# Performance work log

Measured on AMD Instinct MI355X. Metric: run time of the kernel, lower is better.

## Reference

```python
import jax, jax.numpy as jnp
import numpy as np

B, N, OUT = 128, 4096, 64
PHI = (64, 128, 256)
RHO = (256, 128)
FMIN = jnp.finfo(jnp.float32).min


def _linear_params(key, fan_in, fan_out):
    # torch nn.Linear default init: U(-1/sqrt(fan_in), 1/sqrt(fan_in))
    kw, kb = jax.random.split(key)
    bound = 1.0 / np.sqrt(fan_in)
    w = jax.random.uniform(kw, (fan_in, fan_out), jnp.float32, -bound, bound)
    b = jax.random.uniform(kb, (fan_out,), jnp.float32, -bound, bound)
    return w, b


def setup_inputs() -> dict:
    key = jax.random.key(0)
    ks = jax.random.split(key, 8)
    points = jax.random.normal(ks[0], (B, N, 2), jnp.float32)
    lengths = jax.random.randint(ks[1], (B,), 1, N + 1, jnp.int32)
    w1, b1 = _linear_params(ks[2], 2, PHI[0])
    w2, b2 = _linear_params(ks[3], PHI[0], PHI[1])
    w3, b3 = _linear_params(ks[4], PHI[1], PHI[2])
    r1w, r1b = _linear_params(ks[5], PHI[2], RHO[0])
    r2w, r2b = _linear_params(ks[6], RHO[0], RHO[1])
    r3w, r3b = _linear_params(ks[7], RHO[1], OUT)
    return {"points": points, "lengths": lengths,
            "w1": w1, "b1": b1, "w2": w2, "b2": b2, "w3": w3, "b3": b3,
            "r1w": r1w, "r1b": r1b, "r2w": r2w, "r2b": r2b, "r3w": r3w, "r3b": r3b}


def reference(points, lengths, w1, b1, w2, b2, w3, b3, r1w, r1b, r2w, r2b, r3w, r3b):
    # mask[b, n] = n < lengths[b]   (pad_sequence equivalent)
    mask = jnp.arange(N)[None, :] < lengths[:, None]            # [B, N]
    # phi MLP: per-point 2 -> 64 -> 128 -> 256 with ReLU
    h = jax.nn.relu(jnp.einsum('bnd,df->bnf', points, w1) + b1)
    h = jax.nn.relu(jnp.einsum('bnd,df->bnf', h, w2) + b2)
    h = jax.nn.relu(jnp.einsum('bnd,df->bnf', h, w3) + b3)       # [B, N, 256]
    # masked max-pool over points (padding -> dtype min, matching masked_fill)
    h = jnp.where(mask[:, :, None], h, FMIN)
    agg = jnp.max(h, axis=1)                                     # [B, 256]
    # rho MLP: 256 -> 256 -> 128 -> OUT (ReLU on hidden layers only)
    z = jax.nn.relu(agg @ r1w + r1b)
    z = jax.nn.relu(z @ r2w + r2b)
    return z @ r3w + r3b                                         # [B, OUT]
```

## Files before the change

### kernel.cpp

```cpp
#include <hip/hip_runtime.h>
#include <hip/hip_fp16.h>

#define BB   128
#define NN   4096
#define OUTD 64
#define P1   64
#define P2   128
#define P3   256
#define R1   256
#define R2   128
#define CHUNK 64

typedef _Float16 half8 __attribute__((ext_vector_type(8)));
typedef _Float16 half4 __attribute__((ext_vector_type(4)));
typedef float    f32x4 __attribute__((ext_vector_type(4)));

#define AGG_OFF 0
#define W2F_OFF (BB * P3 * 4)
#define W3F_OFF (W2F_OFF + P2 * P1 * 2)

__global__ void prep_kernel(const float* __restrict__ w2, const float* __restrict__ w3,
                            unsigned char* ws) {
  int idx = blockIdx.x * 256 + threadIdx.x;
  if (idx < BB * P3) ((unsigned*)(ws + AGG_OFF))[idx] = 0u;
  _Float16* W2F = (_Float16*)(ws + W2F_OFF);
  _Float16* W3F = (_Float16*)(ws + W3F_OFF);
  if (idx < P1 * P2) {
    int f = idx >> 9, rem = idx & 511, l = rem >> 3, j = rem & 7;
    int mt = f >> 1, ks = f & 1;
    int ch = mt * 16 + (l & 15), k = ks * 32 + (l >> 4) * 8 + j;
    W2F[idx] = (_Float16)w2[k * P2 + ch];
  }
  int i2 = idx - P1 * P2;
  if (i2 >= 0 && i2 < P2 * P3) {
    int f = i2 >> 9, rem = i2 & 511, l = rem >> 3, j = rem & 7;
    int mt = f >> 2, ks = f & 3;
    int ch = mt * 16 + (l & 15), k = ks * 32 + (l >> 4) * 8 + j;
    W3F[i2] = (_Float16)w3[k * P3 + ch];
  }
}

__launch_bounds__(256, 3)
__global__ void phi_kernel(const float* __restrict__ pts, const int* __restrict__ lengths,
                           const float* __restrict__ w1, const float* __restrict__ b1,
                           const float* __restrict__ b2, const float* __restrict__ b3,
                           unsigned char* ws) {
  __shared__ __align__(16) _Float16 sH1[8][CHUNK][8];
  __shared__ __align__(16) _Float16 sH2[16][CHUNK][8];

  int b  = blockIdx.y;
  int c0 = blockIdx.x * CHUNK;
  int len = lengths[b];
  if (c0 >= len) return;
  int v = min(CHUNK, len - c0);

  int t = threadIdx.x;
  int w = t >> 6, l = t & 63;
  int ml = l & 15, q = l >> 4;

  const half8* W2F = (const half8*)(ws + W2F_OFF);
  const half8* W3F = (const half8*)(ws + W3F_OFF);

  half8 a2[2][2];
#pragma unroll
  for (int mt2 = 0; mt2 < 2; ++mt2)
#pragma unroll
    for (int ks = 0; ks < 2; ++ks)
      a2[mt2][ks] = W2F[((w * 2 + mt2) * 2 + ks) * 64 + l];
  half8 a3c[4];
#pragma unroll
  for (int ks = 0; ks < 4; ++ks)
    a3c[ks] = W3F[((w * 4 + 0) * 4 + ks) * 64 + l];

  {
    const float2* Pp = (const float2*)pts + (size_t)b * NN + c0;
    float2 xy = Pp[l];
    half8 h8[2];
#pragma unroll
    for (int j = 0; j < 16; ++j) {
      int jj = w * 16 + j;
      float h = fmaf(xy.y, w1[P1 + jj], fmaf(xy.x, w1[jj], b1[jj]));
      h8[j >> 3][j & 7] = (_Float16)fmaxf(h, 0.f);
    }
    *(half8*)&sH1[w * 2][l][0]     = h8[0];
    *(half8*)&sH1[w * 2 + 1][l][0] = h8[1];
  }
  __syncthreads();

  {
    f32x4 acc2[2][4] = {};
#pragma unroll
    for (int ks = 0; ks < 2; ++ks) {
      half8 bf[4];
#pragma unroll
      for (int nt = 0; nt < 4; ++nt)
        bf[nt] = *(const half8*)&sH1[ks * 4 + q][nt * 16 + ml][0];
#pragma unroll
      for (int mt2 = 0; mt2 < 2; ++mt2)
#pragma unroll
        for (int nt = 0; nt < 4; ++nt)
          acc2[mt2][nt] = __builtin_amdgcn_mfma_f32_16x16x32_f16(
              a2[mt2][ks], bf[nt], acc2[mt2][nt], 0, 0, 0);
    }
#pragma unroll
    for (int mt2 = 0; mt2 < 2; ++mt2) {
      float4 b2v = *(const float4*)&b2[(w * 2 + mt2) * 16 + q * 4];
#pragma unroll
      for (int nt = 0; nt < 4; ++nt) {
        half4 hp;
        hp[0] = (_Float16)fmaxf(acc2[mt2][nt][0] + b2v.x, 0.f);
        hp[1] = (_Float16)fmaxf(acc2[mt2][nt][1] + b2v.y, 0.f);
        hp[2] = (_Float16)fmaxf(acc2[mt2][nt][2] + b2v.z, 0.f);
        hp[3] = (_Float16)fmaxf(acc2[mt2][nt][3] + b2v.w, 0.f);
        *(half4*)&sH2[(w * 2 + mt2) * 2 + (q >> 1)][nt * 16 + ml][(q & 1) * 4] = hp;
      }
    }
  }
  __syncthreads();

  unsigned* aggU = (unsigned*)(ws + AGG_OFF) + b * P3;
  half8 bf3[4][4];
#pragma unroll
  for (int ks = 0; ks < 4; ++ks)
#pragma unroll
    for (int nt = 0; nt < 4; ++nt)
      bf3[ks][nt] = *(const half8*)&sH2[ks * 4 + q][nt * 16 + ml][0];

  for (int s = 0; s < 4; ++s) {
    float4 b3v = *(const float4*)&b3[(w * 4 + s) * 16 + q * 4];
    f32x4 acc3[4] = {};
#pragma unroll
    for (int ks = 0; ks < 4; ++ks)
#pragma unroll
      for (int nt = 0; nt < 4; ++nt)
        acc3[nt] = __builtin_amdgcn_mfma_f32_16x16x32_f16(
            a3c[ks], bf3[ks][nt], acc3[nt], 0, 0, 0);
    if (s < 3) {
#pragma unroll
      for (int ks = 0; ks < 4; ++ks)
        a3c[ks] = W3F[((w * 4 + s + 1) * 4 + ks) * 64 + l];
    }
    float rm[4] = {0.f, 0.f, 0.f, 0.f};
    float bb[4] = {b3v.x, b3v.y, b3v.z, b3v.w};
#pragma unroll
    for (int nt = 0; nt < 4; ++nt) {
      bool ok = (nt * 16 + ml) < v;
#pragma unroll
      for (int r = 0; r < 4; ++r) {
        float val = fmaxf(acc3[nt][r] + bb[r], 0.f);
        if (ok) rm[r] = fmaxf(rm[r], val);
      }
    }
#pragma unroll
    for (int r = 0; r < 4; ++r) {
      float m = rm[r];
      m = fmaxf(m, __shfl_xor(m, 1));
      m = fmaxf(m, __shfl_xor(m, 2));
      m = fmaxf(m, __shfl_xor(m, 4));
      m = fmaxf(m, __shfl_xor(m, 8));
      if (ml == 0)
        atomicMax(&aggU[(w * 4 + s) * 16 + q * 4 + r], __float_as_uint(m));
    }
  }
}

__global__ void rho_kernel(const unsigned char* __restrict__ ws,
                           const float* __restrict__ r1w, const float* __restrict__ r1b,
                           const float* __restrict__ r2w, const float* __restrict__ r2b,
                           const float* __restrict__ r3w, const float* __restrict__ r3b,
                           float* __restrict__ out) {
  __shared__ float sa[R1], sz1[R1], sz2[R2];
  int b = blockIdx.x, t = threadIdx.x;
  const float* agg = (const float*)(ws + AGG_OFF) + b * P3;
  sa[t] = agg[t];
  __syncthreads();
  {
    float p0 = 0.f, p1 = 0.f, p2 = 0.f, p3 = 0.f;
#pragma unroll 8
    for (int k = 0; k < 64; ++k) {
      p0 = fmaf(sa[k],       r1w[k * R1 + t],         p0);
      p1 = fmaf(sa[k + 64],  r1w[(k + 64) * R1 + t],  p1);
      p2 = fmaf(sa[k + 128], r1w[(k + 128) * R1 + t], p2);
      p3 = fmaf(sa[k + 192], r1w[(k + 192) * R1 + t], p3);
    }
    sz1[t] = fmaxf(r1b[t] + ((p0 + p1) + (p2 + p3)), 0.f);
  }
  __syncthreads();
  if (t < R2) {
    float p0 = 0.f, p1 = 0.f, p2 = 0.f, p3 = 0.f;
#pragma unroll 8
    for (int k = 0; k < 64; ++k) {
      p0 = fmaf(sz1[k],       r2w[k * R2 + t],         p0);
      p1 = fmaf(sz1[k + 64],  r2w[(k + 64) * R2 + t],  p1);
      p2 = fmaf(sz1[k + 128], r2w[(k + 128) * R2 + t], p2);
      p3 = fmaf(sz1[k + 192], r2w[(k + 192) * R2 + t], p3);
    }
    sz2[t] = fmaxf(r2b[t] + ((p0 + p1) + (p2 + p3)), 0.f);
  }
  __syncthreads();
  if (t < OUTD) {
    float p0 = 0.f, p1 = 0.f;
#pragma unroll 8
    for (int k = 0; k < 64; ++k) {
      p0 = fmaf(sz2[k],      r3w[k * OUTD + t],        p0);
      p1 = fmaf(sz2[k + 64], r3w[(k + 64) * OUTD + t], p1);
    }
    out[b * OUTD + t] = r3b[t] + p0 + p1;
  }
}

extern "C" void kernel_launch(void* const* d_in, const int* in_sizes, int n_in,
                              void* d_out, int out_size, void* d_ws, size_t ws_size,
                              hipStream_t stream) {
  const float* pts     = (const float*)d_in[0];
  const int*   lengths = (const int*)d_in[1];
  const float* w1  = (const float*)d_in[2];
  const float* b1  = (const float*)d_in[3];
  const float* w2  = (const float*)d_in[4];
  const float* b2  = (const float*)d_in[5];
  const float* w3  = (const float*)d_in[6];
  const float* b3  = (const float*)d_in[7];
  const float* r1w = (const float*)d_in[8];
  const float* r1b = (const float*)d_in[9];
  const float* r2w = (const float*)d_in[10];
  const float* r2b = (const float*)d_in[11];
  const float* r3w = (const float*)d_in[12];
  const float* r3b = (const float*)d_in[13];
  unsigned char* ws = (unsigned char*)d_ws;

  prep_kernel<<<160, 256, 0, stream>>>(w2, w3, ws);
  phi_kernel<<<dim3(NN / CHUNK, BB), 256, 0, stream>>>(pts, lengths, w1, b1, b2, b3, ws);
  rho_kernel<<<BB, 256, 0, stream>>>(ws, r1w, r1b, r2w, r2b, r3w, r3b, (float*)d_out);
}
```

Measured before the change: 142.3 us.

## Process four point chunks per block with software-pipelined layer-1 and W3 prefetch

Each phi block now loops over up to four 64-point chunks instead of one. This amortizes the W2 fragment loads, launch overhead and block setup across more work. Inside the loop, the next chunk's points are loaded and its layer-1 activations computed while the current chunk's layer-3 MFMAs run, and W3 fragments are double-buffered into a second register set. The trade-off is four times fewer blocks (lower parallelism and load balance across ragged lengths), more register pressure from a3n, and an extra barrier per chunk.

```diff
diff --git a/kernel.cpp b/kernel.cpp
--- a/kernel.cpp
+++ b/kernel.cpp
@@ -10,6 +10,7 @@
 #define R1   256
 #define R2   128
 #define CHUNK 64
+#define NCH  4
 
 typedef _Float16 half8 __attribute__((ext_vector_type(8)));
 typedef _Float16 half4 __attribute__((ext_vector_type(4)));
@@ -48,11 +49,12 @@
   __shared__ __align__(16) _Float16 sH1[8][CHUNK][8];
   __shared__ __align__(16) _Float16 sH2[16][CHUNK][8];
 
-  int b  = blockIdx.y;
-  int c0 = blockIdx.x * CHUNK;
-  int len = lengths[b];
-  if (c0 >= len) return;
-  int v = min(CHUNK, len - c0);
+  int b    = blockIdx.y;
+  int base = blockIdx.x * (CHUNK * NCH);
+  int len  = lengths[b];
+  if (base >= len) return;
+  int rem  = len - base;
+  int nch  = min(NCH, (rem + CHUNK - 1) >> 6);
 
   int t = threadIdx.x;
   int w = t >> 6, l = t & 63;
@@ -60,6 +62,7 @@
 
   const half8* W2F = (const half8*)(ws + W2F_OFF);
   const half8* W3F = (const half8*)(ws + W3F_OFF);
+  const float2* Pp = (const float2*)pts + (size_t)b * NN + base;
 
   half8 a2[2][2];
 #pragma unroll
@@ -67,14 +70,15 @@
 #pragma unroll
     for (int ks = 0; ks < 2; ++ks)
       a2[mt2][ks] = W2F[((w * 2 + mt2) * 2 + ks) * 64 + l];
-  half8 a3c[4];
+  half8 a3c[4], a3n[4];
 #pragma unroll
   for (int ks = 0; ks < 4; ++ks)
     a3c[ks] = W3F[((w * 4 + 0) * 4 + ks) * 64 + l];
 
+  float2 xy = Pp[l];
+  unsigned* aggU = (unsigned*)(ws + AGG_OFF) + b * P3;
+
   {
-    const float2* Pp = (const float2*)pts + (size_t)b * NN + c0;
-    float2 xy = Pp[l];
     half8 h8[2];
 #pragma unroll
     for (int j = 0; j < 16; ++j) {
@@ -87,80 +91,104 @@
   }
   __syncthreads();
 
-  {
-    f32x4 acc2[2][4] = {};
-#pragma unroll
-    for (int ks = 0; ks < 2; ++ks) {
-      half8 bf[4];
+  for (int c = 0; c < nch; ++c) {
+    bool more = (c + 1 < nch);
+    if (more) xy = Pp[(c + 1) * CHUNK + l];
+
+    {
+      f32x4 acc2[2][4] = {};
+#pragma unroll
+      for (int ks = 0; ks < 2; ++ks) {
+        half8 bf[4];
+#pragma unroll
+        for (int nt = 0; nt < 4; ++nt)
+          bf[nt] = *(const half8*)&sH1[ks * 4 + q][nt * 16 + ml][0];
+#pragma unroll
+        for (int mt2 = 0; mt2 < 2; ++mt2)
+#pragma unroll
+          for (int nt = 0; nt < 4; ++nt)
+            acc2[mt2][nt] = __builtin_amdgcn_mfma_f32_16x16x32_f16(
+                a2[mt2][ks], bf[nt], acc2[mt2][nt], 0, 0, 0);
+      }
+#pragma unroll
+      for (int mt2 = 0; mt2 < 2; ++mt2) {
+        float4 b2v = *(const float4*)&b2[(w * 2 + mt2) * 16 + q * 4];
+#pragma unroll
+        for (int nt = 0; nt < 4; ++nt) {
+          half4 hp;
+          hp[0] = (_Float16)fmaxf(acc2[mt2][nt][0] + b2v.x, 0.f);
+          hp[1] = (_Float16)fmaxf(acc2[mt2][nt][1] + b2v.y, 0.f);
+          hp[2] = (_Float16)fmaxf(acc2[mt2][nt][2] + b2v.z, 0.f);
+          hp[3] = (_Float16)fmaxf(acc2[mt2][nt][3] + b2v.w, 0.f);
+          *(half4*)&sH2[(w * 2 + mt2) * 2 + (q >> 1)][nt * 16 + ml][(q & 1) * 4] = hp;
+        }
+      }
+    }
+    __syncthreads();
+
+    half8 bf3[4][4];
+#pragma unroll
+    for (int ks = 0; ks < 4; ++ks)
 #pragma unroll
       for (int nt = 0; nt < 4; ++nt)
-        bf[nt] = *(const half8*)&sH1[ks * 4 + q][nt * 16 + ml][0];
-#pragma unroll
-      for (int mt2 = 0; mt2 < 2; ++mt2)
+        bf3[ks][nt] = *(const half8*)&sH2[ks * 4 + q][nt * 16 + ml][0];
+
+    if (more) {
+      half8 h8[2];
+#pragma unroll
+      for (int j = 0; j < 16; ++j) {
+        int jj = w * 16 + j;
+        float h = fmaf(xy.y, w1[P1 + jj], fmaf(xy.x, w1[jj], b1[jj]));
+        h8[j >> 3][j & 7] = (_Float16)fmaxf(h, 0.f);
+      }
+      *(half8*)&sH1[w * 2][l][0]     = h8[0];
+      *(half8*)&sH1[w * 2 + 1][l][0] = h8[1];
+    }
+
+    int v = min(CHUNK, len - base - c * CHUNK);
+#pragma unroll
+    for (int s = 0; s < 4; ++s) {
+      bool pf = (s < 3) || more;
+      if (pf) {
+#pragma unroll
+        for (int ks = 0; ks < 4; ++ks)
+          a3n[ks] = W3F[((w * 4 + ((s + 1) & 3)) * 4 + ks) * 64 + l];
+      }
+      float4 b3v = *(const float4*)&b3[(w * 4 + s) * 16 + q * 4];
+      f32x4 acc3[4] = {};
+#pragma unroll
+      for (int ks = 0; ks < 4; ++ks)
 #pragma unroll
         for (int nt = 0; nt < 4; ++nt)
-          acc2[mt2][nt] = __builtin_amdgcn_mfma_f32_16x16x32_f16(
-              a2[mt2][ks], bf[nt], acc2[mt2][nt], 0, 0, 0);
-    }
-#pragma unroll
-    for (int mt2 = 0; mt2 < 2; ++mt2) {
-      float4 b2v = *(const float4*)&b2[(w * 2 + mt2) * 16 + q * 4];
+          acc3[nt] = __builtin_amdgcn_mfma_f32_16x16x32_f16(
+              a3c[ks], bf3[ks][nt], acc3[nt], 0, 0, 0);
+      float rm[4] = {0.f, 0.f, 0.f, 0.f};
+      float bb[4] = {b3v.x, b3v.y, b3v.z, b3v.w};
 #pragma unroll
       for (int nt = 0; nt < 4; ++nt) {
-        half4 hp;
-        hp[0] = (_Float16)fmaxf(acc2[mt2][nt][0] + b2v.x, 0.f);
-        hp[1] = (_Float16)fmaxf(acc2[mt2][nt][1] + b2v.y, 0.f);
-        hp[2] = (_Float16)fmaxf(acc2[mt2][nt][2] + b2v.z, 0.f);
-        hp[3] = (_Float16)fmaxf(acc2[mt2][nt][3] + b2v.w, 0.f);
-        *(half4*)&sH2[(w * 2 + mt2) * 2 + (q >> 1)][nt * 16 + ml][(q & 1) * 4] = hp;
-      }
-    }
-  }
-  __syncthreads();
-
-  unsigned* aggU = (unsigned*)(ws + AGG_OFF) + b * P3;
-  half8 bf3[4][4];
-#pragma unroll
-  for (int ks = 0; ks < 4; ++ks)
-#pragma unroll
-    for (int nt = 0; nt < 4; ++nt)
-      bf3[ks][nt] = *(const half8*)&sH2[ks * 4 + q][nt * 16 + ml][0];
-
-  for (int s = 0; s < 4; ++s) {
-    float4 b3v = *(const float4*)&b3[(w * 4 + s) * 16 + q * 4];
-    f32x4 acc3[4] = {};
-#pragma unroll
-    for (int ks = 0; ks < 4; ++ks)
-#pragma unroll
-      for (int nt = 0; nt < 4; ++nt)
-        acc3[nt] = __builtin_amdgcn_mfma_f32_16x16x32_f16(
-            a3c[ks], bf3[ks][nt], acc3[nt], 0, 0, 0);
-    if (s < 3) {
-#pragma unroll
-      for (int ks = 0; ks < 4; ++ks)
-        a3c[ks] = W3F[((w * 4 + s + 1) * 4 + ks) * 64 + l];
-    }
-    float rm[4] = {0.f, 0.f, 0.f, 0.f};
-    float bb[4] = {b3v.x, b3v.y, b3v.z, b3v.w};
-#pragma unroll
-    for (int nt = 0; nt < 4; ++nt) {
-      bool ok = (nt * 16 + ml) < v;
+        bool ok = (nt * 16 + ml) < v;
+#pragma unroll
+        for (int r = 0; r < 4; ++r) {
+          float val = fmaxf(acc3[nt][r] + bb[r], 0.f);
+          if (ok) rm[r] = fmaxf(rm[r], val);
+        }
+      }
 #pragma unroll
       for (int r = 0; r < 4; ++r) {
-        float val = fmaxf(acc3[nt][r] + bb[r], 0.f);
-        if (ok) rm[r] = fmaxf(rm[r], val);
-      }
-    }
-#pragma unroll
-    for (int r = 0; r < 4; ++r) {
-      float m = rm[r];
-      m = fmaxf(m, __shfl_xor(m, 1));
-      m = fmaxf(m, __shfl_xor(m, 2));
-      m = fmaxf(m, __shfl_xor(m, 4));
-      m = fmaxf(m, __shfl_xor(m, 8));
-      if (ml == 0)
-        atomicMax(&aggU[(w * 4 + s) * 16 + q * 4 + r], __float_as_uint(m));
-    }
+        float m = rm[r];
+        m = fmaxf(m, __shfl_xor(m, 1));
+        m = fmaxf(m, __shfl_xor(m, 2));
+        m = fmaxf(m, __shfl_xor(m, 4));
+        m = fmaxf(m, __shfl_xor(m, 8));
+        if (ml == 0)
+          atomicMax(&aggU[(w * 4 + s) * 16 + q * 4 + r], __float_as_uint(m));
+      }
+      if (pf) {
+#pragma unroll
+        for (int ks = 0; ks < 4; ++ks) a3c[ks] = a3n[ks];
+      }
+    }
+    __syncthreads();
   }
 }
 
@@ -229,6 +257,6 @@
   unsigned char* ws = (unsigned char*)d_ws;
 
   prep_kernel<<<160, 256, 0, stream>>>(w2, w3, ws);
-  phi_kernel<<<dim3(NN / CHUNK, BB), 256, 0, stream>>>(pts, lengths, w1, b1, b2, b3, ws);
+  phi_kernel<<<dim3(NN / (CHUNK * NCH), BB), 256, 0, stream>>>(pts, lengths, w1, b1, b2, b3, ws);
   rho_kernel<<<BB, 256, 0, stream>>>(ws, r1w, r1b, r2w, r2b, r3w, r3b, (float*)d_out);
 }
```

Result: slower. 265.4 us (+86.5%).

## Make phi kernel persistent per batch with strided chunks and register max accumulation

Applied to the files above, without the earlier changes.

Replaces the one-block-per-chunk grid with a fixed grid of six blocks per batch row. Each block loops over chunks with stride six, keeps the running max in registers across chunks, and issues atomicMax once at the end. It also prefetches the next chunk's points and drops the ReLU on the last layer, since the running max starts at zero. This is meant to cut atomics, block launch overhead and repeated weight loads. In exchange there is more register pressure, and load balance across blocks now depends on the sequence lengths.

```diff
diff --git a/kernel.cpp b/kernel.cpp
--- a/kernel.cpp
+++ b/kernel.cpp
@@ -10,6 +10,9 @@
 #define R1   256
 #define R2   128
 #define CHUNK 64
+#define NCHK (NN / CHUNK)
+#define GPB  6
+#define PGRID (BB * GPB)
 
 typedef _Float16 half8 __attribute__((ext_vector_type(8)));
 typedef _Float16 half4 __attribute__((ext_vector_type(4)));
@@ -48,11 +51,10 @@
   __shared__ __align__(16) _Float16 sH1[8][CHUNK][8];
   __shared__ __align__(16) _Float16 sH2[16][CHUNK][8];
 
-  int b  = blockIdx.y;
-  int c0 = blockIdx.x * CHUNK;
+  int bid = blockIdx.x;
+  int b = bid & (BB - 1), g = bid >> 7;
   int len = lengths[b];
-  if (c0 >= len) return;
-  int v = min(CHUNK, len - c0);
+  if (g * CHUNK >= len) return;
 
   int t = threadIdx.x;
   int w = t >> 6, l = t & 63;
@@ -60,6 +62,8 @@
 
   const half8* W2F = (const half8*)(ws + W2F_OFF);
   const half8* W3F = (const half8*)(ws + W3F_OFF);
+  const float2* Pp = (const float2*)pts + (size_t)b * NN;
+  unsigned* aggU = (unsigned*)(ws + AGG_OFF) + b * P3;
 
   half8 a2[2][2];
 #pragma unroll
@@ -72,88 +76,96 @@
   for (int ks = 0; ks < 4; ++ks)
     a3c[ks] = W3F[((w * 4 + 0) * 4 + ks) * 64 + l];
 
-  {
-    const float2* Pp = (const float2*)pts + (size_t)b * NN + c0;
-    float2 xy = Pp[l];
-    half8 h8[2];
-#pragma unroll
-    for (int j = 0; j < 16; ++j) {
-      int jj = w * 16 + j;
-      float h = fmaf(xy.y, w1[P1 + jj], fmaf(xy.x, w1[jj], b1[jj]));
-      h8[j >> 3][j & 7] = (_Float16)fmaxf(h, 0.f);
-    }
-    *(half8*)&sH1[w * 2][l][0]     = h8[0];
-    *(half8*)&sH1[w * 2 + 1][l][0] = h8[1];
-  }
-  __syncthreads();
-
-  {
-    f32x4 acc2[2][4] = {};
-#pragma unroll
-    for (int ks = 0; ks < 2; ++ks) {
-      half8 bf[4];
+  float2 xy = Pp[g * CHUNK + l];
+
+  float rm[4][4] = {};
+
+  for (int c = g; c * CHUNK < len; c += GPB) {
+    int v = min(CHUNK, len - c * CHUNK);
+
+    {
+      half8 h8[2];
+#pragma unroll
+      for (int j = 0; j < 16; ++j) {
+        int jj = w * 16 + j;
+        float h = fmaf(xy.y, w1[P1 + jj], fmaf(xy.x, w1[jj], b1[jj]));
+        h8[j >> 3][j & 7] = (_Float16)fmaxf(h, 0.f);
+      }
+      *(half8*)&sH1[w * 2][l][0]     = h8[0];
+      *(half8*)&sH1[w * 2 + 1][l][0] = h8[1];
+    }
+    xy = Pp[min(c + GPB, NCHK - 1) * CHUNK + l];
+    __syncthreads();
+
+    {
+      f32x4 acc2[2][4] = {};
+#pragma unroll
+      for (int ks = 0; ks < 2; ++ks) {
+        half8 bf[4];
+#pragma unroll
+        for (int nt = 0; nt < 4; ++nt)
+          bf[nt] = *(const half8*)&sH1[ks * 4 + q][nt * 16 + ml][0];
+#pragma unroll
+        for (int mt2 = 0; mt2 < 2; ++mt2)
+#pragma unroll
+          for (int nt = 0; nt < 4; ++nt)
+            acc2[mt2][nt] = __builtin_amdgcn_mfma_f32_16x16x32_f16(
+                a2[mt2][ks], bf[nt], acc2[mt2][nt], 0, 0, 0);
+      }
+#pragma unroll
+      for (int mt2 = 0; mt2 < 2; ++mt2) {
+        float4 b2v = *(const float4*)&b2[(w * 2 + mt2) * 16 + q * 4];
+#pragma unroll
+        for (int nt = 0; nt < 4; ++nt) {
+          half4 hp;
+          hp[0] = (_Float16)fmaxf(acc2[mt2][nt][0] + b2v.x, 0.f);
+          hp[1] = (_Float16)fmaxf(acc2[mt2][nt][1] + b2v.y, 0.f);
+          hp[2] = (_Float16)fmaxf(acc2[mt2][nt][2] + b2v.z, 0.f);
+          hp[3] = (_Float16)fmaxf(acc2[mt2][nt][3] + b2v.w, 0.f);
+          *(half4*)&sH2[(w * 2 + mt2) * 2 + (q >> 1)][nt * 16 + ml][(q & 1) * 4] = hp;
+        }
+      }
+    }
+    __syncthreads();
+
+    half8 bf3[4][4];
+#pragma unroll
+    for (int ks = 0; ks < 4; ++ks)
 #pragma unroll
       for (int nt = 0; nt < 4; ++nt)
-        bf[nt] = *(const half8*)&sH1[ks * 4 + q][nt * 16 + ml][0];
-#pragma unroll
-      for (int mt2 = 0; mt2 < 2; ++mt2)
+        bf3[ks][nt] = *(const half8*)&sH2[ks * 4 + q][nt * 16 + ml][0];
+
+#pragma unroll
+    for (int s = 0; s < 4; ++s) {
+      float4 b3v = *(const float4*)&b3[(w * 4 + s) * 16 + q * 4];
+      f32x4 acc3[4] = {};
+#pragma unroll
+      for (int ks = 0; ks < 4; ++ks)
 #pragma unroll
         for (int nt = 0; nt < 4; ++nt)
-          acc2[mt2][nt] = __builtin_amdgcn_mfma_f32_16x16x32_f16(
-              a2[mt2][ks], bf[nt], acc2[mt2][nt], 0, 0, 0);
-    }
-#pragma unroll
-    for (int mt2 = 0; mt2 < 2; ++mt2) {
-      float4 b2v = *(const float4*)&b2[(w * 2 + mt2) * 16 + q * 4];
+          acc3[nt] = __builtin_amdgcn_mfma_f32_16x16x32_f16(
+              a3c[ks], bf3[ks][nt], acc3[nt], 0, 0, 0);
+#pragma unroll
+      for (int ks = 0; ks < 4; ++ks)
+        a3c[ks] = W3F[((w * 4 + ((s + 1) & 3)) * 4 + ks) * 64 + l];
+      float bb[4] = {b3v.x, b3v.y, b3v.z, b3v.w};
 #pragma unroll
       for (int nt = 0; nt < 4; ++nt) {
-        half4 hp;
-        hp[0] = (_Float16)fmaxf(acc2[mt2][nt][0] + b2v.x, 0.f);
-        hp[1] = (_Float16)fmaxf(acc2[mt2][nt][1] + b2v.y, 0.f);
-        hp[2] = (_Float16)fmaxf(acc2[mt2][nt][2] + b2v.z, 0.f);
-        hp[3] = (_Float16)fmaxf(acc2[mt2][nt][3] + b2v.w, 0.f);
-        *(half4*)&sH2[(w * 2 + mt2) * 2 + (q >> 1)][nt * 16 + ml][(q & 1) * 4] = hp;
-      }
-    }
-  }
-  __syncthreads();
-
-  unsigned* aggU = (unsigned*)(ws + AGG_OFF) + b * P3;
-  half8 bf3[4][4];
-#pragma unroll
-  for (int ks = 0; ks < 4; ++ks)
-#pragma unroll
-    for (int nt = 0; nt < 4; ++nt)
-      bf3[ks][nt] = *(const half8*)&sH2[ks * 4 + q][nt * 16 + ml][0];
-
-  for (int s = 0; s < 4; ++s) {
-    float4 b3v = *(const float4*)&b3[(w * 4 + s) * 16 + q * 4];
-    f32x4 acc3[4] = {};
-#pragma unroll
-    for (int ks = 0; ks < 4; ++ks)
-#pragma unroll
-      for (int nt = 0; nt < 4; ++nt)
-        acc3[nt] = __builtin_amdgcn_mfma_f32_16x16x32_f16(
-            a3c[ks], bf3[ks][nt], acc3[nt], 0, 0, 0);
-    if (s < 3) {
-#pragma unroll
-      for (int ks = 0; ks < 4; ++ks)
-        a3c[ks] = W3F[((w * 4 + s + 1) * 4 + ks) * 64 + l];
-    }
-    float rm[4] = {0.f, 0.f, 0.f, 0.f};
-    float bb[4] = {b3v.x, b3v.y, b3v.z, b3v.w};
-#pragma unroll
-    for (int nt = 0; nt < 4; ++nt) {
-      bool ok = (nt * 16 + ml) < v;
-#pragma unroll
-      for (int r = 0; r < 4; ++r) {
-        float val = fmaxf(acc3[nt][r] + bb[r], 0.f);
-        if (ok) rm[r] = fmaxf(rm[r], val);
-      }
-    }
+        bool ok = (nt * 16 + ml) < v;
+#pragma unroll
+        for (int r = 0; r < 4; ++r) {
+          float val = acc3[nt][r] + bb[r];
+          if (ok) rm[s][r] = fmaxf(rm[s][r], val);
+        }
+      }
+    }
+  }
+
+#pragma unroll
+  for (int s = 0; s < 4; ++s)
 #pragma unroll
     for (int r = 0; r < 4; ++r) {
-      float m = rm[r];
+      float m = rm[s][r];
       m = fmaxf(m, __shfl_xor(m, 1));
       m = fmaxf(m, __shfl_xor(m, 2));
       m = fmaxf(m, __shfl_xor(m, 4));
@@ -161,7 +173,6 @@
       if (ml == 0)
         atomicMax(&aggU[(w * 4 + s) * 16 + q * 4 + r], __float_as_uint(m));
     }
-  }
 }
 
 __global__ void rho_kernel(const unsigned char* __restrict__ ws,
@@ -229,6 +240,6 @@
   unsigned char* ws = (unsigned char*)d_ws;
 
   prep_kernel<<<160, 256, 0, stream>>>(w2, w3, ws);
-  phi_kernel<<<dim3(NN / CHUNK, BB), 256, 0, stream>>>(pts, lengths, w1, b1, b2, b3, ws);
+  phi_kernel<<<PGRID, 256, 0, stream>>>(pts, lengths, w1, b1, b2, b3, ws);
   rho_kernel<<<BB, 256, 0, stream>>>(ws, r1w, r1b, r2w, r2b, r3w, r3b, (float*)d_out);
 }
```

Result: slower. 244.1 us (+71.6%).
